# Optimization experiments

Measured on AMD Instinct MI355X. Metric: run time of the kernel, lower is better.

The kernel has to match this reference:

```python
import jax, jax.numpy as jnp
import numpy as np

NUM_CLASSES = 97  # vocab size; SOS token id == NUM_CLASSES
D = 512   # in_planes (xDim)
S = 512   # sDim (GRU hidden)
A = 512   # attDim == emdDim
T = 25    # max_len_labels == encoder length L
B = 2048  # batch


def setup_inputs() -> dict:
    key = jax.random.key(0)
    ks = jax.random.split(key, 15)
    r = lambda k, shp: jax.random.normal(k, shp, jnp.float32) * 0.05
    return dict(
        x=jax.random.normal(ks[0], (B, T, D), jnp.float32),
        targets=jax.random.randint(ks[1], (2, B, T), 0, NUM_CLASSES),  # (fwd, reversed)
        Wx=r(ks[2], (2, D, A)), bx=r(ks[3], (2, A)),
        Ws=r(ks[4], (2, S, A)), bs=r(ks[5], (2, A)),
        wv=r(ks[6], (2, A)), wvb=r(ks[7], (2,)),
        emb=r(ks[8], (2, NUM_CLASSES + 1, A)),
        Wih=r(ks[9], (2, 3 * S, D + A)), bih=r(ks[10], (2, 3 * S)),
        Whh=r(ks[11], (2, 3 * S, S)), bhh=r(ks[12], (2, 3 * S)),
        Wfc=r(ks[13], (2, NUM_CLASSES, S)), bfc=r(ks[14], (2, NUM_CLASSES)),
    )


def _decode(x, targets, Wx, bx, Ws, bs, wv, wvb, emb, Wih, bih, Whh, bhh, Wfc, bfc):
    """One DecoderUnit unrolled over T steps (teacher forcing). x: [B,L,D]."""
    Bn = x.shape[0]
    # xEmbed is step-invariant -> hoist out of the recurrence
    xProj = jnp.einsum('bld,da->bla', x, Wx) + bx  # [B,L,A]
    y0 = jnp.full((Bn, 1), NUM_CLASSES, dtype=targets.dtype)  # SOS at step 0
    y_seq = jnp.concatenate([y0, targets[:, :-1]], axis=1)     # [B,T]

    def step(s, y_prev):
        # Bahdanau attention
        sProj = s @ Ws + bs                                  # [B,A]
        e = jnp.tanh(sProj[:, None, :] + xProj) @ wv + wvb   # [B,L]
        alpha = jax.nn.softmax(e, axis=1)
        ctx = jnp.einsum('bl,bld->bd', alpha, x)             # [B,D]
        # single-step GRU (PyTorch gate convention: r, z, n)
        gin = jnp.concatenate([emb[y_prev], ctx], axis=1)    # [B, A+D]
        gi = gin @ Wih.T + bih                               # [B,3S]
        gh = s @ Whh.T + bhh
        ir, iz, inn = jnp.split(gi, 3, axis=1)
        hr, hz, hn = jnp.split(gh, 3, axis=1)
        r = jax.nn.sigmoid(ir + hr)
        z = jax.nn.sigmoid(iz + hz)
        n = jnp.tanh(inn + r * hn)
        s_new = (1.0 - z) * n + z * s
        return s_new, s_new @ Wfc.T + bfc                    # logits [B,C]

    s0 = jnp.zeros((Bn, S), x.dtype)
    _, outs = jax.lax.scan(step, s0, jnp.swapaxes(y_seq, 0, 1))  # [T,B,C]
    return jnp.swapaxes(outs, 0, 1)  # [B,T,C]


def reference(x, targets, Wx, bx, Ws, bs, wv, wvb, emb, Wih, bih, Whh, bhh, Wfc, bfc):
    # vmap over the 2 decoders (forward / reverse); x shared
    f = jax.vmap(_decode, in_axes=(None, 0) + (0,) * 13)
    return f(x, targets, Wx, bx, Ws, bs, wv, wvb, emb, Wih, bih, Whh, bhh, Wfc, bfc)  # [2,B,T,C]
```

## Files before the change

kernel.cpp:

```cpp
#include <hip/hip_runtime.h>
#include <hip/hip_fp16.h>

#define B_ 2048
#define T_ 25
#define CL_ 97

typedef float f32x4 __attribute__((ext_vector_type(4)));
typedef float f32x2 __attribute__((ext_vector_type(2)));
typedef _Float16 f16x8 __attribute__((ext_vector_type(8)));
typedef _Float16 f16x2 __attribute__((ext_vector_type(2)));

#define DI static __device__ __forceinline__

DI float fast_tanh(float x) { return 1.0f - 2.0f / (__expf(2.0f * x) + 1.0f); }
DI float fast_sigm(float x) { return 1.0f / (1.0f + __expf(-x)); }

DI void gl16(const void* g, void* l) {
    __builtin_amdgcn_global_load_lds((const __attribute__((address_space(1))) void*)g,
                                     (__attribute__((address_space(3))) void*)l, 16, 0, 0);
}


__global__ void k_convx(const float* __restrict__ x, _Float16* __restrict__ xh, int n8) {
    int i = blockIdx.x * 256 + threadIdx.x;
    if (i >= n8) return;
    const f32x4 v0 = *(const f32x4*)(x + (long long)i * 8);
    const f32x4 v1 = *(const f32x4*)(x + (long long)i * 8 + 4);
    f16x8 o;
    o[0] = (_Float16)v0[0]; o[1] = (_Float16)v0[1]; o[2] = (_Float16)v0[2]; o[3] = (_Float16)v0[3];
    o[4] = (_Float16)v1[0]; o[5] = (_Float16)v1[1]; o[6] = (_Float16)v1[2]; o[7] = (_Float16)v1[3];
    *(f16x8*)(xh + (long long)i * 8) = o;
}

__global__ void k_pack_w1(const float* __restrict__ Ws, const float* __restrict__ Whh,
                          const float* __restrict__ Wfc, const float* __restrict__ bs,
                          const float* __restrict__ bhh, const float* __restrict__ bfc,
                          _Float16* __restrict__ w1, float* __restrict__ b1) {
    int idx = blockIdx.x * 256 + threadIdx.x;
    if (idx >= 2 * 2176 * 64) return;
    const int k8 = idx & 63;
    const int n  = (idx >> 6) % 2176;
    const int g  = (idx >> 6) / 2176;
    const int k0 = k8 * 8;
    f16x8 o;
    if (n < 512) {
        const float* p = Ws + (long long)g * 512 * 512 + (long long)k0 * 512 + n;
        #pragma unroll
        for (int i = 0; i < 8; ++i) o[i] = (_Float16)p[(long long)i * 512];
    } else if (n < 2048) {
        const float* p = Whh + (long long)g * 1536 * 512 + (long long)(n - 512) * 512 + k0;
        #pragma unroll
        for (int i = 0; i < 8; ++i) o[i] = (_Float16)p[i];
    } else if (n < 2048 + CL_) {
        const float* p = Wfc + (long long)g * CL_ * 512 + (long long)(n - 2048) * 512 + k0;
        #pragma unroll
        for (int i = 0; i < 8; ++i) o[i] = (_Float16)p[i];
    } else {
        #pragma unroll
        for (int i = 0; i < 8; ++i) o[i] = (_Float16)0.0f;
    }
    *(f16x8*)(w1 + ((long long)g * 2176 + n) * 512 + k0) = o;
    if (k8 == 0) {
        float bv = (n < 512) ? bs[g * 512 + n]
                 : (n < 2048) ? bhh[g * 1536 + (n - 512)]
                 : (n < 2048 + CL_) ? bfc[g * CL_ + (n - 2048)] : 0.0f;
        b1[g * 2176 + n] = bv;
    }
}

__global__ void k_pack_w2(const float* __restrict__ Wih, _Float16* __restrict__ w2,
                          _Float16* __restrict__ w2e) {
    int idx = blockIdx.x * 256 + threadIdx.x;
    if (idx >= 2 * 1536 * 64) return;
    const int k8 = idx & 63;
    const int n  = (idx >> 6) % 1536;
    const int g  = (idx >> 6) / 1536;
    const int k0 = k8 * 8;
    const float* p = Wih + (long long)g * 1536 * 1024 + (long long)n * 1024;
    f16x8 o, oe;
    #pragma unroll
    for (int i = 0; i < 8; ++i) { o[i] = (_Float16)p[512 + k0 + i]; oe[i] = (_Float16)p[k0 + i]; }
    *(f16x8*)(w2  + ((long long)g * 1536 + n) * 512 + k0) = o;
    *(f16x8*)(w2e + ((long long)g * 1536 + n) * 512 + k0) = oe;
}

__global__ void k_pack_wx(const float* __restrict__ Wx, _Float16* __restrict__ wx) {
    int idx = blockIdx.x * 256 + threadIdx.x;
    if (idx >= 2 * 512 * 64) return;
    const int k8 = idx & 63;
    const int n  = (idx >> 6) & 511;
    const int g  = (idx >> 6) >> 9;
    const int k0 = k8 * 8;
    const float* p = Wx + (long long)g * 512 * 512 + (long long)k0 * 512 + n;
    f16x8 o;
    #pragma unroll
    for (int i = 0; i < 8; ++i) o[i] = (_Float16)p[(long long)i * 512];
    *(f16x8*)(wx + ((long long)g * 512 + n) * 512 + k0) = o;
}

__global__ void k_pack_emb(const float* __restrict__ emb, _Float16* __restrict__ embh) {
    int i = blockIdx.x * 256 + threadIdx.x;
    if (i >= 2 * 128 * 64) return;
    const int k8 = i & 63;
    const int y  = (i >> 6) & 127;
    const int g  = i >> 13;
    f16x8 o;
    if (y < 98) {
        const float* p = emb + (long long)(g * 98 + y) * 512 + k8 * 8;
        #pragma unroll
        for (int j = 0; j < 8; ++j) o[j] = (_Float16)p[j];
    } else {
        #pragma unroll
        for (int j = 0; j < 8; ++j) o[j] = (_Float16)0.0f;
    }
    *(f16x8*)(embh + (long long)(g * 128 + y) * 512 + k8 * 8) = o;
}

__global__ __launch_bounds__(256) void gemm_bt(
    const _Float16* __restrict__ A, long long aG,
    const _Float16* __restrict__ B, long long bG,
    float* __restrict__ Cf, _Float16* __restrict__ Ch,
    long long cG, int ldc,
    const float* __restrict__ bias, int biasG,
    int nblk_off, int n_split,
    float* __restrict__ lout, int lcols, int lldc)
{
    __shared__ _Float16 As[128 * 64];
    __shared__ _Float16 Bs[128 * 64];
    const int gx = gridDim.x, nwg = gx * gridDim.y;
    const int o = blockIdx.y * gx + blockIdx.x;
    const int q = nwg >> 3, r = nwg & 7;
    const int xcd = o & 7, ii = o >> 3;
    const int nn = (xcd < r ? xcd * (q + 1) : r * (q + 1) + (xcd - r) * q) + ii;
    const int bx = nn % gx, by = nn / gx;

    const int g  = blockIdx.z;
    const int m0 = by * 128;
    const int n0 = (bx + nblk_off) * 128;
    const _Float16* Ag = A + (long long)g * aG + (long long)m0 * 512;
    const _Float16* Bg = B + (long long)g * bG + (long long)n0 * 512;
    const int tid  = threadIdx.x;
    const int lane = tid & 63, w = tid >> 6;
    const int wr = w >> 1, wc = w & 1;
    const int lr = lane & 15, kg = lane >> 4;
    const int srow = lane >> 3;
    const int scol = (((lane & 7) ^ srow) * 8);

    f32x4 acc[4][4];
    #pragma unroll
    for (int m = 0; m < 4; ++m)
        #pragma unroll
        for (int n = 0; n < 4; ++n) acc[m][n] = (f32x4)0.0f;

    #pragma unroll
    for (int kt = 0; kt < 8; ++kt) {
        const int k0 = kt * 64;
        __syncthreads();
        #pragma unroll
        for (int cc = 0; cc < 4; ++cc) {
            const int rr = w * 32 + cc * 8;
            gl16(Ag + (long long)(rr + srow) * 512 + k0 + scol, &As[rr * 64]);
            gl16(Bg + (long long)(rr + srow) * 512 + k0 + scol, &Bs[rr * 64]);
        }
        __syncthreads();
        #pragma unroll
        for (int kk = 0; kk < 2; ++kk) {
            f16x8 af[4], bf[4];
            #pragma unroll
            for (int m = 0; m < 4; ++m) {
                const int R = wr * 64 + m * 16 + lr;
                af[m] = *(const f16x8*)&As[R * 64 + (((kk * 4 + kg) ^ (R & 7)) * 8)];
            }
            #pragma unroll
            for (int n = 0; n < 4; ++n) {
                const int R = wc * 64 + n * 16 + lr;
                bf[n] = *(const f16x8*)&Bs[R * 64 + (((kk * 4 + kg) ^ (R & 7)) * 8)];
            }
            #pragma unroll
            for (int m = 0; m < 4; ++m)
                #pragma unroll
                for (int n = 0; n < 4; ++n)
                    acc[m][n] = __builtin_amdgcn_mfma_f32_16x16x32_f16(af[m], bf[n], acc[m][n], 0, 0, 0);
        }
    }

    #pragma unroll
    for (int n = 0; n < 4; ++n) {
        const int col = n0 + wc * 64 + n * 16 + lr;
        const float bb = bias ? bias[g * biasG + col] : 0.0f;
        if (col < n_split) {
            #pragma unroll
            for (int m = 0; m < 4; ++m) {
                const int row = m0 + wr * 64 + m * 16 + kg * 4;
                #pragma unroll
                for (int i = 0; i < 4; ++i) {
                    const long long off = (long long)g * cG + (long long)(row + i) * ldc + col;
                    const float v = acc[m][n][i] + bb;
                    if (Ch) Ch[off] = (_Float16)v; else Cf[off] = v;
                }
            }
        } else if (lout != nullptr) {
            const int c = col - n_split;
            if (c < lcols) {
                #pragma unroll
                for (int m = 0; m < 4; ++m) {
                    const int row = m0 + wr * 64 + m * 16 + kg * 4;
                    #pragma unroll
                    for (int i = 0; i < 4; ++i)
                        lout[(long long)(g * B_ + row + i) * lldc + c] = acc[m][n][i] + bb;
                }
            }
        }
    }
}

__global__ __launch_bounds__(256) void k_att(
    const _Float16* __restrict__ Yh,
    const _Float16* __restrict__ xpj,
    const _Float16* __restrict__ xh,
    const float* __restrict__ wv,
    _Float16* __restrict__ ctxh)
{
    const int b = blockIdx.x;
    const int tid = threadIdx.x, lane = tid & 63, w = tid >> 6;
    __shared__ float eL[2][28];
    __shared__ float red[2][4][512];
    const int a0 = lane * 8;

    #pragma unroll
    for (int g = 0; g < 2; ++g) {
        const _Float16* sp = Yh + (long long)(g * B_ + b) * 2048;
        const f16x8 spv = *(const f16x8*)(sp + a0);
        const float* wvg = wv + g * 512;
        const f32x4 wv0 = *(const f32x4*)(wvg + a0);
        const f32x4 wv1 = *(const f32x4*)(wvg + a0 + 4);
        const _Float16* xpb = xpj + (long long)(g * B_ + b) * 25 * 512;
        for (int l = w; l < 25; l += 4) {
            const f16x8 xv = *(const f16x8*)(xpb + l * 512 + a0);
            float part = 0.0f;
            #pragma unroll
            for (int i = 0; i < 4; ++i) {
                part += fast_tanh((float)spv[i]     + (float)xv[i])     * wv0[i];
                part += fast_tanh((float)spv[4 + i] + (float)xv[4 + i]) * wv1[i];
            }
            #pragma unroll
            for (int off = 32; off > 0; off >>= 1) part += __shfl_xor(part, off);
            if (lane == 0) eL[g][l] = part;
        }
    }
    __syncthreads();

    float al0[25], al1[25];
    float m0 = -1e30f, m1 = -1e30f;
    #pragma unroll
    for (int l = 0; l < 25; ++l) { m0 = fmaxf(m0, eL[0][l]); m1 = fmaxf(m1, eL[1][l]); }
    float ss0 = 0.0f, ss1 = 0.0f;
    #pragma unroll
    for (int l = 0; l < 25; ++l) {
        al0[l] = __expf(eL[0][l] - m0); ss0 += al0[l];
        al1[l] = __expf(eL[1][l] - m1); ss1 += al1[l];
    }
    const float inv0 = 1.0f / ss0, inv1 = 1.0f / ss1;

    float c0[8], c1[8];
    #pragma unroll
    for (int j = 0; j < 8; ++j) { c0[j] = 0.0f; c1[j] = 0.0f; }
    const _Float16* xb = xh + (long long)b * 25 * 512;
    #pragma unroll
    for (int l = 0; l < 25; ++l) {
        if ((l & 3) == w) {
            const f16x8 xv = *(const f16x8*)(xb + l * 512 + a0);
            #pragma unroll
            for (int j = 0; j < 8; ++j) {
                const float xf = (float)xv[j];
                c0[j] += al0[l] * xf;
                c1[j] += al1[l] * xf;
            }
        }
    }
    f32x4 p;
    #pragma unroll
    for (int h = 0; h < 2; ++h) {
        #pragma unroll
        for (int i = 0; i < 4; ++i) p[i] = c0[h * 4 + i] * inv0;
        *(f32x4*)&red[0][w][a0 + h * 4] = p;
        #pragma unroll
        for (int i = 0; i < 4; ++i) p[i] = c1[h * 4 + i] * inv1;
        *(f32x4*)&red[1][w][a0 + h * 4] = p;
    }
    __syncthreads();

    const int c = tid * 2;
    f32x2 s0 = {0.0f, 0.0f}, s1 = {0.0f, 0.0f};
    #pragma unroll
    for (int ww = 0; ww < 4; ++ww) {
        s0 += *(const f32x2*)&red[0][ww][c];
        s1 += *(const f32x2*)&red[1][ww][c];
    }
    f16x2 o0, o1;
    o0[0] = (_Float16)s0[0]; o0[1] = (_Float16)s0[1];
    o1[0] = (_Float16)s1[0]; o1[1] = (_Float16)s1[1];
    *(f16x2*)(ctxh + (long long)b * 512 + c) = o0;
    *(f16x2*)(ctxh + (long long)(B_ + b) * 512 + c) = o1;
}

__global__ void k_gate(const _Float16* __restrict__ Yh,
                       const _Float16* __restrict__ Y2h,
                       const float* __restrict__ eW,
                       const int* __restrict__ tgt,
                       float* __restrict__ s32, _Float16* __restrict__ sh, int t)
{
    const int idx = blockIdx.x * 256 + threadIdx.x;
    if (idx >= 2 * B_ * 256) return;
    const int jp = (idx & 255) * 2;
    const int b  = (idx >> 8) & (B_ - 1);
    const int g  = idx >> 19;
    const int y  = (t == 0) ? CL_ : tgt[(g * B_ + b) * T_ + t - 1];
    const float*    ew = eW  + (long long)(g * 128 + y) * 1536;
    const _Float16* y2 = Y2h + (long long)(g * B_ + b) * 1536;
    const _Float16* yy = Yh  + (long long)(g * B_ + b) * 2048;
    const f32x2 ewr = *(const f32x2*)(ew + jp);
    const f32x2 ewz = *(const f32x2*)(ew + 512 + jp);
    const f32x2 ewn = *(const f32x2*)(ew + 1024 + jp);
    const f16x2 y2r = *(const f16x2*)(y2 + jp);
    const f16x2 y2z = *(const f16x2*)(y2 + 512 + jp);
    const f16x2 y2n = *(const f16x2*)(y2 + 1024 + jp);
    const f16x2 ghr = *(const f16x2*)(yy + 512 + jp);
    const f16x2 ghz = *(const f16x2*)(yy + 1024 + jp);
    const f16x2 ghn = *(const f16x2*)(yy + 1536 + jp);
    const long long si = (long long)(g * B_ + b) * 512 + jp;
    const f32x2 so = *(const f32x2*)(s32 + si);
    f32x2 sn;
    f16x2 snh;
    #pragma unroll
    for (int i = 0; i < 2; ++i) {
        const float r  = fast_sigm(ewr[i] + (float)y2r[i] + (float)ghr[i]);
        const float z  = fast_sigm(ewz[i] + (float)y2z[i] + (float)ghz[i]);
        const float nn = fast_tanh(ewn[i] + (float)y2n[i] + r * (float)ghn[i]);
        sn[i]  = (1.0f - z) * nn + z * so[i];
        snh[i] = (_Float16)sn[i];
    }
    *(f32x2*)(s32 + si) = sn;
    *(f16x2*)(sh + si) = snh;
}

extern "C" void kernel_launch(void* const* d_in, const int* in_sizes, int n_in,
                              void* d_out, int out_size, void* d_ws, size_t ws_size,
                              hipStream_t stream)
{
    (void)in_sizes; (void)n_in; (void)out_size;
    const float* x   = (const float*)d_in[0];
    const int*   tgt = (const int*)d_in[1];
    const float* Wx  = (const float*)d_in[2];
    const float* bx  = (const float*)d_in[3];
    const float* Wsm = (const float*)d_in[4];
    const float* bs  = (const float*)d_in[5];
    const float* wv  = (const float*)d_in[6];
    const float* emb = (const float*)d_in[8];
    const float* Wih = (const float*)d_in[9];
    const float* bih = (const float*)d_in[10];
    const float* Whh = (const float*)d_in[11];
    const float* bhh = (const float*)d_in[12];
    const float* Wfc = (const float*)d_in[13];
    const float* bfc = (const float*)d_in[14];
    float* out = (float*)d_out;

    char* base = (char*)d_ws;
    size_t off = 0;
    auto alloc = [&](size_t bytes) -> void* {
        void* r = base + off;
        off = (off + bytes + 255) & ~(size_t)255;
        return r;
    };
    _Float16* xh   = (_Float16*)alloc((size_t)B_ * T_ * 512 * 2);
    _Float16* xpj  = (_Float16*)alloc((size_t)2 * B_ * T_ * 512 * 2);
    _Float16* w1   = (_Float16*)alloc((size_t)2 * 2176 * 512 * 2);
    _Float16* w2   = (_Float16*)alloc((size_t)2 * 1536 * 512 * 2);
    _Float16* w2e  = (_Float16*)alloc((size_t)2 * 1536 * 512 * 2);
    _Float16* wx   = (_Float16*)alloc((size_t)2 * 512 * 512 * 2);
    _Float16* embh = (_Float16*)alloc((size_t)2 * 128 * 512 * 2);
    float*    b1   = (float*)alloc((size_t)2 * 2176 * 4);
    float*    eW   = (float*)alloc((size_t)2 * 128 * 1536 * 4);
    float*    s32  = (float*)alloc((size_t)2 * B_ * 512 * 4);
    _Float16* sh   = (_Float16*)alloc((size_t)2 * B_ * 512 * 2);
    _Float16* ctx  = (_Float16*)alloc((size_t)2 * B_ * 512 * 2);
    _Float16* Yh   = (_Float16*)alloc((size_t)2 * B_ * 2048 * 2);
    _Float16* Y2h  = (_Float16*)alloc((size_t)2 * B_ * 1536 * 2);
    if (off > ws_size) return;

    hipMemsetAsync(s32, 0, (size_t)2 * B_ * 512 * 4, stream);
    hipMemsetAsync(sh,  0, (size_t)2 * B_ * 512 * 2, stream);

    k_convx   <<<12800, 256, 0, stream>>>(x, xh, (B_ * T_ * 512) / 8);
    k_pack_w1 <<<1088, 256, 0, stream>>>(Wsm, Whh, Wfc, bs, bhh, bfc, w1, b1);
    k_pack_w2 <<<768, 256, 0, stream>>>(Wih, w2, w2e);
    k_pack_wx <<<256, 256, 0, stream>>>(Wx, wx);
    k_pack_emb<<<64, 256, 0, stream>>>(emb, embh);

    gemm_bt<<<dim3(12, 1, 2), 256, 0, stream>>>(
        embh, 128ll * 512, w2e, 1536ll * 512, eW, nullptr,
        128ll * 1536, 1536, bih, 1536, 0, 1 << 30, nullptr, 0, 0);

    gemm_bt<<<dim3(4, 400, 2), 256, 0, stream>>>(
        xh, 0ll, wx, 512ll * 512, nullptr, xpj, (long long)B_ * T_ * 512, 512,
        bx, 512, 0, 1 << 30, nullptr, 0, 0);

    for (int t = 0; t < T_; ++t) {
        gemm_bt<<<dim3(t > 0 ? 17 : 16, 16, 2), 256, 0, stream>>>(
            sh, (long long)B_ * 512, w1, 2176ll * 512, nullptr, Yh,
            (long long)B_ * 2048, 2048, b1, 2176, 0, 2048,
            t > 0 ? out + (long long)(t - 1) * CL_ : nullptr, CL_, T_ * CL_);
        k_att<<<dim3(B_, 1, 1), 256, 0, stream>>>(Yh, xpj, xh, wv, ctx);
        gemm_bt<<<dim3(12, 16, 2), 256, 0, stream>>>(
            ctx, (long long)B_ * 512, w2, 1536ll * 512, nullptr, Y2h,
            (long long)B_ * 1536, 1536, nullptr, 0, 0, 1 << 30, nullptr, 0, 0);
        k_gate<<<4096, 256, 0, stream>>>(Yh, Y2h, eW, tgt, s32, sh, t);
    }
    gemm_bt<<<dim3(1, 16, 2), 256, 0, stream>>>(
        sh, (long long)B_ * 512, w1, 2176ll * 512, nullptr, Yh,
        (long long)B_ * 2048, 2048, b1, 2176, 16, 2048,
        out + 24ll * CL_, CL_, T_ * CL_);
}
```

Before: 2.675 ms.

## Fuse GRU gate into ctx GEMM via last-block counter and coalesce f16 epilogue

Replaces the separate ctx×Wih GEMM and elementwise gate kernel with one kernel. Each 128-row block of the gate is finished by the last workgroup to complete its row tile, detected with an atomic counter. This removes one launch per timestep and lets the gate read Y2h while it is likely still in cache. The f16 GEMM epilogue is also changed to stage through LDS and write 16-byte coalesced stores. The trade-off is that the gate work for a row tile runs serially in one workgroup (256 threads doing 128 rows), which risks a tail imbalance, and it adds threadfence and atomic overhead.

Result: slower. 7.464 ms (+179.0%).

```diff
diff --git a/kernel.cpp b/kernel.cpp
--- a/kernel.cpp
+++ b/kernel.cpp
@@ -116,6 +116,75 @@
     *(f16x8*)(embh + (long long)(g * 128 + y) * 512 + k8 * 8) = o;
 }
 
+DI void xcd_remap(int gx, int gy, int& bx, int& by) {
+    const int nwg = gx * gy;
+    const int o = blockIdx.y * gx + blockIdx.x;
+    const int q = nwg >> 3, r = nwg & 7;
+    const int xcd = o & 7, ii = o >> 3;
+    const int nn = (xcd < r ? xcd * (q + 1) : r * (q + 1) + (xcd - r) * q) + ii;
+    bx = nn % gx; by = nn / gx;
+}
+
+#define GEMM_CORE(Ag, Bg, acc)                                                          \
+    _Float16* As = (_Float16*)smem;                                                     \
+    _Float16* Bs = (_Float16*)(smem + 16384);                                           \
+    _Pragma("unroll")                                                                   \
+    for (int kt = 0; kt < 8; ++kt) {                                                    \
+        const int k0 = kt * 64;                                                         \
+        __syncthreads();                                                                \
+        _Pragma("unroll")                                                               \
+        for (int cc = 0; cc < 4; ++cc) {                                                \
+            const int rr = w * 32 + cc * 8;                                             \
+            gl16(Ag + (long long)(rr + srow) * 512 + k0 + scol, &As[rr * 64]);          \
+            gl16(Bg + (long long)(rr + srow) * 512 + k0 + scol, &Bs[rr * 64]);          \
+        }                                                                               \
+        __syncthreads();                                                                \
+        _Pragma("unroll")                                                               \
+        for (int kk = 0; kk < 2; ++kk) {                                                \
+            f16x8 af[4], bf[4];                                                         \
+            _Pragma("unroll")                                                           \
+            for (int m = 0; m < 4; ++m) {                                               \
+                const int R = wr * 64 + m * 16 + lr;                                    \
+                af[m] = *(const f16x8*)&As[R * 64 + (((kk * 4 + kg) ^ (R & 7)) * 8)];   \
+            }                                                                           \
+            _Pragma("unroll")                                                           \
+            for (int n = 0; n < 4; ++n) {                                               \
+                const int R = wc * 64 + n * 16 + lr;                                    \
+                bf[n] = *(const f16x8*)&Bs[R * 64 + (((kk * 4 + kg) ^ (R & 7)) * 8)];   \
+            }                                                                           \
+            _Pragma("unroll")                                                           \
+            for (int m = 0; m < 4; ++m)                                                 \
+                _Pragma("unroll")                                                       \
+                for (int n = 0; n < 4; ++n)                                             \
+                    acc[m][n] = __builtin_amdgcn_mfma_f32_16x16x32_f16(af[m], bf[n], acc[m][n], 0, 0, 0); \
+        }                                                                               \
+    }
+
+#define EPI_F16_COALESCED(Chp, ldc_, base_)                                             \
+    {                                                                                   \
+        __syncthreads();                                 \
+        _Float16* Cs = (_Float16*)smem;                                                 \
+        _Pragma("unroll")                                                               \
+        for (int n = 0; n < 4; ++n) {                                                   \
+            const int cl = wc * 64 + n * 16 + lr;                                       \
+            _Pragma("unroll")                                                           \
+            for (int m = 0; m < 4; ++m) {                                               \
+                const int rbase = wr * 64 + m * 16 + kg * 4;                            \
+                _Pragma("unroll")                                                       \
+                for (int i = 0; i < 4; ++i)                                             \
+                    Cs[(rbase + i) * 128 + cl] = (_Float16)(acc[m][n][i] + bb[n]);      \
+            }                                                                           \
+        }                                                                               \
+        __syncthreads();                                                                \
+        const int c8 = (tid & 15) * 8;                                                  \
+        _Pragma("unroll")                                                               \
+        for (int r8 = 0; r8 < 8; ++r8) {                                                \
+            const int rr = r8 * 16 + (tid >> 4);                                        \
+            *(f16x8*)(Chp + (base_) + (long long)(m0 + rr) * (ldc_) + n0 + c8) =        \
+                *(const f16x8*)&Cs[rr * 128 + c8];                                      \
+        }                                                                               \
+    }
+
 __global__ __launch_bounds__(256) void gemm_bt(
     const _Float16* __restrict__ A, long long aG,
     const _Float16* __restrict__ B, long long bG,
@@ -125,15 +194,8 @@
     int nblk_off, int n_split,
     float* __restrict__ lout, int lcols, int lldc)
 {
-    __shared__ _Float16 As[128 * 64];
-    __shared__ _Float16 Bs[128 * 64];
-    const int gx = gridDim.x, nwg = gx * gridDim.y;
-    const int o = blockIdx.y * gx + blockIdx.x;
-    const int q = nwg >> 3, r = nwg & 7;
-    const int xcd = o & 7, ii = o >> 3;
-    const int nn = (xcd < r ? xcd * (q + 1) : r * (q + 1) + (xcd - r) * q) + ii;
-    const int bx = nn % gx, by = nn / gx;
-
+    __shared__ __align__(16) char smem[32768];
+    int bx, by; xcd_remap(gridDim.x, gridDim.y, bx, by);
     const int g  = blockIdx.z;
     const int m0 = by * 128;
     const int n0 = (bx + nblk_off) * 128;
@@ -152,52 +214,27 @@
         #pragma unroll
         for (int n = 0; n < 4; ++n) acc[m][n] = (f32x4)0.0f;
 
-    #pragma unroll
-    for (int kt = 0; kt < 8; ++kt) {
-        const int k0 = kt * 64;
-        __syncthreads();
-        #pragma unroll
-        for (int cc = 0; cc < 4; ++cc) {
-            const int rr = w * 32 + cc * 8;
-            gl16(Ag + (long long)(rr + srow) * 512 + k0 + scol, &As[rr * 64]);
-            gl16(Bg + (long long)(rr + srow) * 512 + k0 + scol, &Bs[rr * 64]);
-        }
-        __syncthreads();
-        #pragma unroll
-        for (int kk = 0; kk < 2; ++kk) {
-            f16x8 af[4], bf[4];
-            #pragma unroll
-            for (int m = 0; m < 4; ++m) {
-                const int R = wr * 64 + m * 16 + lr;
-                af[m] = *(const f16x8*)&As[R * 64 + (((kk * 4 + kg) ^ (R & 7)) * 8)];
-            }
-            #pragma unroll
-            for (int n = 0; n < 4; ++n) {
-                const int R = wc * 64 + n * 16 + lr;
-                bf[n] = *(const f16x8*)&Bs[R * 64 + (((kk * 4 + kg) ^ (R & 7)) * 8)];
-            }
-            #pragma unroll
-            for (int m = 0; m < 4; ++m)
-                #pragma unroll
-                for (int n = 0; n < 4; ++n)
-                    acc[m][n] = __builtin_amdgcn_mfma_f32_16x16x32_f16(af[m], bf[n], acc[m][n], 0, 0, 0);
-        }
-    }
-
+    GEMM_CORE(Ag, Bg, acc)
+
+    float bb[4];
+    #pragma unroll
+    for (int n = 0; n < 4; ++n)
+        bb[n] = bias ? bias[g * biasG + n0 + wc * 64 + n * 16 + lr] : 0.0f;
+
+    if (Ch && n0 + 128 <= n_split) {
+        EPI_F16_COALESCED(Ch, ldc, (long long)g * cG)
+        return;
+    }
     #pragma unroll
     for (int n = 0; n < 4; ++n) {
         const int col = n0 + wc * 64 + n * 16 + lr;
-        const float bb = bias ? bias[g * biasG + col] : 0.0f;
         if (col < n_split) {
             #pragma unroll
             for (int m = 0; m < 4; ++m) {
                 const int row = m0 + wr * 64 + m * 16 + kg * 4;
                 #pragma unroll
-                for (int i = 0; i < 4; ++i) {
-                    const long long off = (long long)g * cG + (long long)(row + i) * ldc + col;
-                    const float v = acc[m][n][i] + bb;
-                    if (Ch) Ch[off] = (_Float16)v; else Cf[off] = v;
-                }
+                for (int i = 0; i < 4; ++i)
+                    Cf[(long long)g * cG + (long long)(row + i) * ldc + col] = acc[m][n][i] + bb[n];
             }
         } else if (lout != nullptr) {
             const int c = col - n_split;
@@ -207,10 +244,95 @@
                     const int row = m0 + wr * 64 + m * 16 + kg * 4;
                     #pragma unroll
                     for (int i = 0; i < 4; ++i)
-                        lout[(long long)(g * B_ + row + i) * lldc + c] = acc[m][n][i] + bb;
+                        lout[(long long)(g * B_ + row + i) * lldc + c] = acc[m][n][i] + bb[n];
                 }
             }
         }
+    }
+}
+
+__global__ __launch_bounds__(256) void k2_gate(
+    const _Float16* __restrict__ ctx,
+    const _Float16* __restrict__ w2,
+    _Float16* __restrict__ Y2h,
+    const _Float16* __restrict__ Yh,
+    const float* __restrict__ eW,
+    const int* __restrict__ tgt,
+    float* __restrict__ s32, _Float16* __restrict__ sh,
+    int* __restrict__ cnt, int t)
+{
+    __shared__ __align__(16) char smem[32768];
+    __shared__ int lastFlag;
+    int bx, by; xcd_remap(gridDim.x, gridDim.y, bx, by);
+    const int g  = blockIdx.z;
+    const int m0 = by * 128;
+    const int n0 = bx * 128;
+    const _Float16* Ag = ctx + (long long)g * B_ * 512 + (long long)m0 * 512;
+    const _Float16* Bg = w2  + (long long)g * 1536 * 512 + (long long)n0 * 512;
+    const int tid  = threadIdx.x;
+    const int lane = tid & 63, w = tid >> 6;
+    const int wr = w >> 1, wc = w & 1;
+    const int lr = lane & 15, kg = lane >> 4;
+    const int srow = lane >> 3;
+    const int scol = (((lane & 7) ^ srow) * 8);
+
+    f32x4 acc[4][4];
+    #pragma unroll
+    for (int m = 0; m < 4; ++m)
+        #pragma unroll
+        for (int n = 0; n < 4; ++n) acc[m][n] = (f32x4)0.0f;
+
+    GEMM_CORE(Ag, Bg, acc)
+
+    float bb[4] = {0.0f, 0.0f, 0.0f, 0.0f};
+    EPI_F16_COALESCED(Y2h, 1536, (long long)g * B_ * 1536)
+
+    __threadfence();
+    if (tid == 0) {
+        const int old = atomicAdd(&cnt[g * 16 + by], 1);
+        lastFlag = (((old + 1) % 12) == 0);
+    }
+    __syncthreads();
+    if (!lastFlag) return;
+    __threadfence();
+
+    const int r   = tid >> 1;
+    const int row = m0 + r;
+    const int jb  = (tid & 1) * 256;
+    const int y   = (t == 0) ? CL_ : tgt[(g * B_ + row) * T_ + t - 1];
+    const float*    ew = eW  + (long long)(g * 128 + y) * 1536;
+    const _Float16* y2 = Y2h + (long long)(g * B_ + row) * 1536;
+    const _Float16* gh = Yh  + (long long)(g * B_ + row) * 2048;
+    float*    sr = s32 + (long long)(g * B_ + row) * 512;
+    _Float16* sp = sh  + (long long)(g * B_ + row) * 512;
+    for (int j0 = 0; j0 < 256; j0 += 8) {
+        const int j = jb + j0;
+        const f16x8 yr = *(const f16x8*)(y2 + j);
+        const f16x8 yz = *(const f16x8*)(y2 + 512 + j);
+        const f16x8 yn = *(const f16x8*)(y2 + 1024 + j);
+        const f16x8 hr = *(const f16x8*)(gh + 512 + j);
+        const f16x8 hz = *(const f16x8*)(gh + 1024 + j);
+        const f16x8 hn = *(const f16x8*)(gh + 1536 + j);
+        f16x8 snh;
+        #pragma unroll
+        for (int h = 0; h < 2; ++h) {
+            const f32x4 er = *(const f32x4*)(ew + j + h * 4);
+            const f32x4 ez = *(const f32x4*)(ew + 512 + j + h * 4);
+            const f32x4 en = *(const f32x4*)(ew + 1024 + j + h * 4);
+            f32x4 so = *(const f32x4*)(sr + j + h * 4);
+            f32x4 sn;
+            #pragma unroll
+            for (int i = 0; i < 4; ++i) {
+                const int e = h * 4 + i;
+                const float rr = fast_sigm(er[i] + (float)yr[e] + (float)hr[e]);
+                const float zz = fast_sigm(ez[i] + (float)yz[e] + (float)hz[e]);
+                const float nn = fast_tanh(en[i] + (float)yn[e] + rr * (float)hn[e]);
+                sn[i] = (1.0f - zz) * nn + zz * so[i];
+                snh[e] = (_Float16)sn[i];
+            }
+            *(f32x4*)(sr + j + h * 4) = sn;
+        }
+        *(f16x8*)(sp + j) = snh;
     }
 }
 
@@ -302,46 +424,6 @@
     o1[0] = (_Float16)s1[0]; o1[1] = (_Float16)s1[1];
     *(f16x2*)(ctxh + (long long)b * 512 + c) = o0;
     *(f16x2*)(ctxh + (long long)(B_ + b) * 512 + c) = o1;
-}
-
-__global__ void k_gate(const _Float16* __restrict__ Yh,
-                       const _Float16* __restrict__ Y2h,
-                       const float* __restrict__ eW,
-                       const int* __restrict__ tgt,
-                       float* __restrict__ s32, _Float16* __restrict__ sh, int t)
-{
-    const int idx = blockIdx.x * 256 + threadIdx.x;
-    if (idx >= 2 * B_ * 256) return;
-    const int jp = (idx & 255) * 2;
-    const int b  = (idx >> 8) & (B_ - 1);
-    const int g  = idx >> 19;
-    const int y  = (t == 0) ? CL_ : tgt[(g * B_ + b) * T_ + t - 1];
-    const float*    ew = eW  + (long long)(g * 128 + y) * 1536;
-    const _Float16* y2 = Y2h + (long long)(g * B_ + b) * 1536;
-    const _Float16* yy = Yh  + (long long)(g * B_ + b) * 2048;
-    const f32x2 ewr = *(const f32x2*)(ew + jp);
-    const f32x2 ewz = *(const f32x2*)(ew + 512 + jp);
-    const f32x2 ewn = *(const f32x2*)(ew + 1024 + jp);
-    const f16x2 y2r = *(const f16x2*)(y2 + jp);
-    const f16x2 y2z = *(const f16x2*)(y2 + 512 + jp);
-    const f16x2 y2n = *(const f16x2*)(y2 + 1024 + jp);
-    const f16x2 ghr = *(const f16x2*)(yy + 512 + jp);
-    const f16x2 ghz = *(const f16x2*)(yy + 1024 + jp);
-    const f16x2 ghn = *(const f16x2*)(yy + 1536 + jp);
-    const long long si = (long long)(g * B_ + b) * 512 + jp;
-    const f32x2 so = *(const f32x2*)(s32 + si);
-    f32x2 sn;
-    f16x2 snh;
-    #pragma unroll
-    for (int i = 0; i < 2; ++i) {
-        const float r  = fast_sigm(ewr[i] + (float)y2r[i] + (float)ghr[i]);
-        const float z  = fast_sigm(ewz[i] + (float)y2z[i] + (float)ghz[i]);
-        const float nn = fast_tanh(ewn[i] + (float)y2n[i] + r * (float)ghn[i]);
-        sn[i]  = (1.0f - z) * nn + z * so[i];
-        snh[i] = (_Float16)sn[i];
-    }
-    *(f32x2*)(s32 + si) = sn;
-    *(f16x2*)(sh + si) = snh;
 }
 
 extern "C" void kernel_launch(void* const* d_in, const int* in_sizes, int n_in,
@@ -381,15 +463,17 @@
     _Float16* embh = (_Float16*)alloc((size_t)2 * 128 * 512 * 2);
     float*    b1   = (float*)alloc((size_t)2 * 2176 * 4);
     float*    eW   = (float*)alloc((size_t)2 * 128 * 1536 * 4);
+    const size_t zero0 = off;
     float*    s32  = (float*)alloc((size_t)2 * B_ * 512 * 4);
     _Float16* sh   = (_Float16*)alloc((size_t)2 * B_ * 512 * 2);
+    int*      cnt  = (int*)alloc((size_t)2 * 16 * 4);
+    const size_t zero1 = off;
     _Float16* ctx  = (_Float16*)alloc((size_t)2 * B_ * 512 * 2);
     _Float16* Yh   = (_Float16*)alloc((size_t)2 * B_ * 2048 * 2);
     _Float16* Y2h  = (_Float16*)alloc((size_t)2 * B_ * 1536 * 2);
     if (off > ws_size) return;
 
-    hipMemsetAsync(s32, 0, (size_t)2 * B_ * 512 * 4, stream);
-    hipMemsetAsync(sh,  0, (size_t)2 * B_ * 512 * 2, stream);
+    hipMemsetAsync(base + zero0, 0, zero1 - zero0, stream);
 
     k_convx   <<<12800, 256, 0, stream>>>(x, xh, (B_ * T_ * 512) / 8);
     k_pack_w1 <<<1088, 256, 0, stream>>>(Wsm, Whh, Wfc, bs, bhh, bfc, w1, b1);
@@ -411,10 +495,8 @@
             (long long)B_ * 2048, 2048, b1, 2176, 0, 2048,
             t > 0 ? out + (long long)(t - 1) * CL_ : nullptr, CL_, T_ * CL_);
         k_att<<<dim3(B_, 1, 1), 256, 0, stream>>>(Yh, xpj, xh, wv, ctx);
-        gemm_bt<<<dim3(12, 16, 2), 256, 0, stream>>>(
-            ctx, (long long)B_ * 512, w2, 1536ll * 512, nullptr, Y2h,
-            (long long)B_ * 1536, 1536, nullptr, 0, 0, 1 << 30, nullptr, 0, 0);
-        k_gate<<<4096, 256, 0, stream>>>(Yh, Y2h, eW, tgt, s32, sh, t);
+        k2_gate<<<dim3(12, 16, 2), 256, 0, stream>>>(
+            ctx, w2, Y2h, Yh, eW, tgt, s32, sh, cnt, t);
     }
     gemm_bt<<<dim3(1, 16, 2), 256, 0, stream>>>(
         sh, (long long)B_ * 512, w1, 2176ll * 512, nullptr, Yh,
```
